# Kernel tuning notes

Measured on AMD Instinct MI355X. Metric: run time of the kernel, lower is better.

Reference implementation:

```python
import jax, jax.numpy as jnp
import numpy as np

B, C, H, W = 4, 1024, 14, 14
L = 80          # num labels / graph nodes
WD = 300        # word embedding dim
INTER = 1024    # semantic intermediary dim
OUT = 2048      # output_dim
TIME_STEP = 3


def setup_inputs() -> dict:
    key = jax.random.key(0)
    ks = jax.random.split(key, 24)
    s = 0.02  # weight scale to keep gates/tanh in sane range
    return {
        "img_feature_map": jax.random.normal(ks[0], (B, C, H, W), jnp.float32),
        "word_embedding": jax.random.normal(ks[1], (L, WD), jnp.float32),
        "adjacency": jax.random.uniform(ks[2], (L, L), jnp.float32) / L,
        "fc1_w": jax.random.normal(ks[3], (INTER, C), jnp.float32) * s,
        "fc2_w": jax.random.normal(ks[4], (INTER, WD), jnp.float32) * s,
        "fc3_w": jax.random.normal(ks[5], (INTER, INTER), jnp.float32) * s,
        "fc3_b": jnp.zeros((INTER,), jnp.float32),
        "fca_w": jax.random.normal(ks[6], (1, INTER), jnp.float32) * s,
        "fca_b": jnp.zeros((1,), jnp.float32),
        "w3": jax.random.normal(ks[7], (C, 2 * C), jnp.float32) * s,
        "b3": jnp.zeros((C,), jnp.float32),
        "u3": jax.random.normal(ks[8], (C, C), jnp.float32) * s,
        "u3b": jnp.zeros((C,), jnp.float32),
        "w4": jax.random.normal(ks[9], (C, 2 * C), jnp.float32) * s,
        "b4": jnp.zeros((C,), jnp.float32),
        "w5": jax.random.normal(ks[10], (C, 2 * C), jnp.float32) * s,
        "b5": jnp.zeros((C,), jnp.float32),
        "u5": jax.random.normal(ks[11], (C, C), jnp.float32) * s,
        "u5b": jnp.zeros((C,), jnp.float32),
        "fco_w": jax.random.normal(ks[12], (OUT, 2 * C), jnp.float32) * s,
        "fco_b": jnp.zeros((OUT,), jnp.float32),
    }


def _semantic(fmap, word_emb, fc1_w, fc2_w, fc3_w, fc3_b, fca_w, fca_b):
    # Faithful to torch: view(-1, C) on a contiguous (B,C,H,W) tensor is a raw
    # row-major reinterpret (NOT a BHWC transpose). jnp.reshape matches.
    b, c, h, w = fmap.shape
    x = fmap.reshape(-1, c)                                   # (B*H*W, C)
    f_wh = x @ fc1_w.T                                        # (N, INTER)
    f_wd = word_emb @ fc2_w.T                                 # (L, INTER)
    lb = jnp.tanh(f_wh[:, None, :] * f_wd[None, :, :])        # (N, L, INTER)
    lb = lb @ fc3_w.T + fc3_b                                 # (N, L, INTER)
    coeff = lb @ fca_w.T + fca_b                              # (N, L, 1)
    coeff = coeff.reshape(b, L, h * w)                        # torch .view semantics
    coeff = jax.nn.softmax(coeff, axis=2)
    coeff = coeff.reshape(b, h, w, L)
    fmap_bhwc = fmap.reshape(b, h, w, c)                      # raw reinterpret, as torch
    return jnp.einsum('bhwl,bhwc->blc', coeff, fmap_bhwc)     # (B, L, C)


def _ggnn(nodes, adj, w3, b3, u3, u3b, w4, b4, w5, b5, u5, u5b):
    for _ in range(TIME_STEP):
        a = jnp.einsum('nm,bmd->bnd', adj, nodes)             # in == out matrix
        av = jnp.concatenate([a, a], axis=-1)                 # (B, L, 2C)
        u3x = nodes @ u3.T + u3b
        z = jax.nn.sigmoid(av @ w3.T + b3 + u3x)
        r = jax.nn.sigmoid(av @ w4.T + b4 + u3x)              # torch bug: reuses fc_eq3_u
        hcand = jnp.tanh(av @ w5.T + b5 + (r * nodes) @ u5.T + u5b)
        nodes = (1.0 - z) * nodes + z * hcand
    return nodes


def reference(img_feature_map, word_embedding, adjacency,
              fc1_w, fc2_w, fc3_w, fc3_b, fca_w, fca_b,
              w3, b3, u3, u3b, w4, b4, w5, b5, u5, u5b,
              fco_w, fco_b):
    g = _semantic(img_feature_map, word_embedding,
                  fc1_w, fc2_w, fc3_w, fc3_b, fca_w, fca_b)   # (B, L, C)
    nodes = _ggnn(g, adjacency, w3, b3, u3, u3b, w4, b4, w5, b5, u5, u5b)
    feat = jnp.concatenate([nodes, g], axis=-1)               # (B, L, 2C)
    out = jnp.tanh(feat @ fco_w.T + fco_b)                    # (B, L, OUT)
    return out
```

## Files before the change

kernel.cpp:

```cpp
#include <hip/hip_runtime.h>
#include <hip/hip_bf16.h>

#define LL 80
#define NPIX 784
#define PBATCH 15680

#define DI __device__ __forceinline__

typedef short s8v __attribute__((ext_vector_type(8)));
typedef short short4v __attribute__((ext_vector_type(4)));
typedef float f32x4 __attribute__((ext_vector_type(4)));

DI float b2f(__hip_bfloat16 x) { return __bfloat162float(x); }
DI float s2f(short h) { return __uint_as_float(((unsigned int)(unsigned short)h) << 16); }

DI short f2b(float x) {
    unsigned int b = __float_as_uint(x);
    b += 0x7fffu + ((b >> 16) & 1u);
    return (short)(b >> 16);
}

template <int F> DI float LD(const void* p, int i) {
    if (F) return ((const float*)p)[i];
    return b2f(((const __hip_bfloat16*)p)[i]);
}

DI float fast_tanh(float x) {
    float e = __expf(2.0f * x);
    return 1.0f - 2.0f / (e + 1.0f);
}
DI float fast_sigmoid(float x) { return 1.0f / (1.0f + __expf(-x)); }

__global__ __launch_bounds__(256) void detect_dtype(const void* probe, int n, int* flag) {
    __shared__ int bad;
    if (threadIdx.x == 0) bad = 0;
    __syncthreads();
    int c = 0;
    for (int i = threadIdx.x; i < n; i += 256) {
        float v = b2f(((const __hip_bfloat16*)probe)[i]);
        if (!(fabsf(v) < 1000.0f)) c++;
    }
    if (c) atomicAdd(&bad, c);
    __syncthreads();
    if (threadIdx.x == 0) *flag = (bad > 8) ? 1 : 0;
}

DI void cvt_part(int f, const void* src, short* __restrict__ dst, int blk, int n) {
    int i0 = (blk * 256 + threadIdx.x) * 4;
    if (i0 >= n) return;
    if (f) {
        float4 v = *(const float4*)((const float*)src + i0);
        short4v o = { f2b(v.x), f2b(v.y), f2b(v.z), f2b(v.w) };
        *(short4v*)(dst + i0) = o;
    } else {
        *(short4v*)(dst + i0) = *(const short4v*)((const short*)src + i0);
    }
}

DI void wcat_part(int f, const void* w3, const void* w4, const void* w5, const void* u3,
                  short* __restrict__ wcat, int blk) {
    int i0 = (blk * 256 + threadIdx.x) * 4;
    int nr = i0 >> 10, k = i0 & 1023;
    int j = nr >> 10, r = nr & 1023;
    const void* W = (j == 0) ? w3 : (j == 1) ? w4 : (j == 2) ? w5 : u3;
    float4 v;
    if (j < 3) {
        if (f) {
            float4 x = *(const float4*)((const float*)W + r * 2048 + k);
            float4 y = *(const float4*)((const float*)W + r * 2048 + 1024 + k);
            v.x = x.x + y.x; v.y = x.y + y.y; v.z = x.z + y.z; v.w = x.w + y.w;
        } else {
            const short* Ws = (const short*)W;
            short4v x = *(const short4v*)(Ws + r * 2048 + k);
            short4v y = *(const short4v*)(Ws + r * 2048 + 1024 + k);
            v.x = s2f(x.x) + s2f(y.x); v.y = s2f(x.y) + s2f(y.y);
            v.z = s2f(x.z) + s2f(y.z); v.w = s2f(x.w) + s2f(y.w);
        }
    } else {
        if (f) v = *(const float4*)((const float*)W + r * 1024 + k);
        else {
            short4v x = *(const short4v*)((const short*)W + r * 1024 + k);
            v.x = s2f(x.x); v.y = s2f(x.y); v.z = s2f(x.z); v.w = s2f(x.w);
        }
    }
    short4v o = { f2b(v.x), f2b(v.y), f2b(v.z), f2b(v.w) };
    *(short4v*)(wcat + i0) = o;
}

template <int F>
DI void prep_u_part(const void* fc3_w, const void* fc3_b,
                    const void* fca_w, const void* fca_b,
                    float* u, float* c0, float* red, int blk) {
    if (blk < 4) {
        int k = blk * 256 + threadIdx.x;
        float acc = 0.f;
        for (int j = 0; j < 1024; j++)
            acc += LD<F>(fca_w, j) * LD<F>(fc3_w, j * 1024 + k);
        u[k] = acc;
    } else {
        float acc = 0.f;
        for (int j = threadIdx.x; j < 1024; j += 256)
            acc += LD<F>(fc3_b, j) * LD<F>(fca_w, j);
        red[threadIdx.x] = acc;
        __syncthreads();
        for (int s = 128; s > 0; s >>= 1) {
            if (threadIdx.x < s) red[threadIdx.x] += red[threadIdx.x + s];
            __syncthreads();
        }
        if (threadIdx.x == 0) *c0 = red[0] + LD<F>(fca_b, 0);
    }
}

template <int F>
DI void fc2_part(float* lds, const void* word, const void* fc2_w, float* C, int bx, int by) {
    float* As = lds;
    float* Ws2 = lds + 1088;
    const int tid = threadIdx.x;
    const int tx = tid & 15, ty = tid >> 4;
    const int m0 = by * 64, n0 = bx * 64;
    const int M = 80, K = 300;
    float acc[4][4] = {};

    for (int k0 = 0; k0 < K; k0 += 16) {
#pragma unroll
        for (int i = 0; i < 4; i++) {
            int idx = tid + i * 256;
            int kk = idx & 15, mm = idx >> 4;
            int m = m0 + mm, k = k0 + kk;
            As[kk * 68 + mm] = (m < M && k < K) ? LD<F>(word, m * 300 + k) : 0.f;
        }
#pragma unroll
        for (int i = 0; i < 4; i++) {
            int idx = tid + i * 256;
            int kk = idx & 15, nn = idx >> 4;
            int n = n0 + nn, k = k0 + kk;
            Ws2[kk * 68 + nn] = (k < K) ? LD<F>(fc2_w, n * 300 + k) : 0.f;
        }
        __syncthreads();
#pragma unroll
        for (int kk = 0; kk < 16; kk++) {
            float4 av = *(const float4*)(&As[kk * 68 + ty * 4]);
            float4 wv = *(const float4*)(&Ws2[kk * 68 + tx * 4]);
            float a4[4] = {av.x, av.y, av.z, av.w};
            float w4[4] = {wv.x, wv.y, wv.z, wv.w};
#pragma unroll
            for (int i = 0; i < 4; i++)
#pragma unroll
                for (int j = 0; j < 4; j++)
                    acc[i][j] += a4[i] * w4[j];
        }
        __syncthreads();
    }

    for (int i = 0; i < 4; i++) {
        int m = m0 + ty * 4 + i;
        if (m >= M) continue;
        for (int j = 0; j < 4; j++)
            C[m * 1024 + n0 + tx * 4 + j] = acc[i][j];
    }
}

__global__ __launch_bounds__(256) void mega_prep(
    const int* flag,
    const void* fmap, const void* fc1_w, const void* u5w,
    const void* w3, const void* w4, const void* w5, const void* u3,
    const void* fc3_w, const void* fc3_b, const void* fca_w, const void* fca_b,
    const void* word, const void* fc2_w,
    short* fmap_b, short* fc1w_b, short* u5w_b, short* wcat_b,
    float* u, float* c0, float* f_wd) {
    __shared__ float lds[2176];
    int f = *flag;
    int bid = blockIdx.x;
    if      (bid < 784)  cvt_part(f, fmap,  fmap_b, bid,        802816);
    else if (bid < 1808) cvt_part(f, fc1_w, fc1w_b, bid - 784,  1048576);
    else if (bid < 2832) cvt_part(f, u5w,   u5w_b,  bid - 1808, 1048576);
    else if (bid < 6928) wcat_part(f, w3, w4, w5, u3, wcat_b, bid - 2832);
    else if (bid < 6933) {
        if (f) prep_u_part<1>(fc3_w, fc3_b, fca_w, fca_b, u, c0, lds, bid - 6928);
        else   prep_u_part<0>(fc3_w, fc3_b, fca_w, fca_b, u, c0, lds, bid - 6928);
    } else {
        int r = bid - 6933;
        if (f) fc2_part<1>(lds, word, fc2_w, f_wd, r & 15, r >> 4);
        else   fc2_part<0>(lds, word, fc2_w, f_wd, r & 15, r >> 4);
    }
}

__global__ __launch_bounds__(256) void cvt_k(const int* flag, const void* src,
                                             short* __restrict__ dst, int n) {
    cvt_part(*flag, src, dst, blockIdx.x, n);
}

DI void mcore_b(const short* __restrict__ A, int lda,
                const short* __restrict__ B, int ldb,
                float* __restrict__ C, int ldc,
                int M, int kb, int ke, int m0, int n0) {
    __shared__ short As[4][64][8];
    __shared__ short Ws[4][64][8];
    const int tid = threadIdx.x;
    const int wv = tid >> 6, lane = tid & 63;
    const int mA = tid & 63, qA = tid >> 6;
    f32x4 acc[4] = {};

    for (int k0 = kb; k0 < ke; k0 += 32) {
        s8v va = {0,0,0,0,0,0,0,0};
        int gm = m0 + mA;
        if (gm < M) va = *(const s8v*)(A + gm * lda + k0 + 8 * qA);
        *(s8v*)&As[mA >> 4][(mA & 15) | (qA << 4)][0] = va;
        s8v vb = *(const s8v*)(B + (n0 + mA) * ldb + k0 + 8 * qA);
        *(s8v*)&Ws[mA >> 4][(mA & 15) | (qA << 4)][0] = vb;
        __syncthreads();
        s8v af = *(const s8v*)&As[wv][lane][0];
#pragma unroll
        for (int nf = 0; nf < 4; nf++) {
            s8v bf = *(const s8v*)&Ws[nf][lane][0];
            acc[nf] = __builtin_amdgcn_mfma_f32_16x16x32_bf16(af, bf, acc[nf], 0, 0, 0);
        }
        __syncthreads();
    }

    const int q = lane >> 4, cc = lane & 15;
#pragma unroll
    for (int nf = 0; nf < 4; nf++) {
        int n = n0 + 16 * nf + cc;
#pragma unroll
        for (int r = 0; r < 4; r++) {
            int m = m0 + 16 * wv + q * 4 + r;
            if (m < M) C[m * ldc + n] = acc[nf][r];
        }
    }
}

__global__ __launch_bounds__(256) void mfma_fc1(
    const short* __restrict__ fmap_b, const short* __restrict__ fc1w_b,
    float* __restrict__ fhP) {
    int z = blockIdx.z;
    mcore_b(fmap_b, 1024, fc1w_b, 1024, fhP + z * 802816, 1024,
            NPIX, z * 512, z * 512 + 512, blockIdx.y * 64, blockIdx.x * 64);
}

__global__ __launch_bounds__(256) void mfma_gate(
    const short* __restrict__ a_b, const short* __restrict__ nodes_b,
    const short* __restrict__ wcat_b, float* __restrict__ gP) {
    int z = blockIdx.z;
    const short* A = (blockIdx.x >= 48) ? nodes_b : a_b;
    mcore_b(A, 1024, wcat_b, 1024, gP + z * 1310720, 4096,
            320, z * 512, z * 512 + 512, blockIdx.y * 64, blockIdx.x * 64);
}

__global__ __launch_bounds__(256) void mfma_u5(
    const short* __restrict__ rn_b, const short* __restrict__ u5w_b,
    float* __restrict__ u5P) {
    int z = blockIdx.z;
    mcore_b(rn_b, 1024, u5w_b, 1024, u5P + z * 327680, 1024,
            320, z * 256, z * 256 + 256, blockIdx.y * 64, blockIdx.x * 64);
}

__global__ __launch_bounds__(256) void mfma_fin(
    const short* __restrict__ nodes_b, const short* __restrict__ g_b,
    const short* __restrict__ fcow_b, float* __restrict__ finP) {
    int z = blockIdx.z;
    const short* A = z ? (g_b - 1024) : nodes_b;
    mcore_b(A, 1024, fcow_b, 2048, finP + z * 655360, 2048,
            320, z * 1024, z * 1024 + 1024, blockIdx.y * 64, blockIdx.x * 64);
}

__global__ void fin_combine(const int* flag, const float* __restrict__ finP,
                            const void* fco_b, void* out, int n) {
    int i4 = (blockIdx.x * 256 + threadIdx.x) * 4;
    if (i4 >= n) return;
    int c = i4 & 2047;
    float4 p0 = *(const float4*)(finP + i4);
    float4 p1 = *(const float4*)(finP + 655360 + i4);
    int f = *flag;
    float v0 = fast_tanh(p0.x + p1.x + (f ? LD<1>(fco_b, c)   : LD<0>(fco_b, c)));
    float v1 = fast_tanh(p0.y + p1.y + (f ? LD<1>(fco_b, c+1) : LD<0>(fco_b, c+1)));
    float v2 = fast_tanh(p0.z + p1.z + (f ? LD<1>(fco_b, c+2) : LD<0>(fco_b, c+2)));
    float v3 = fast_tanh(p0.w + p1.w + (f ? LD<1>(fco_b, c+3) : LD<0>(fco_b, c+3)));
    if (f) {
        float4 o = {v0, v1, v2, v3};
        *(float4*)((float*)out + i4) = o;
    } else {
        short4v o = { f2b(v0), f2b(v1), f2b(v2), f2b(v3) };
        *(short4v*)((short*)out + i4) = o;
    }
}

__global__ __launch_bounds__(256) void coeff_kernel(
    const float* __restrict__ fhP, const float* __restrict__ f_wd,
    const float* __restrict__ u, const float* __restrict__ c0p,
    float* __restrict__ s) {
    int n = blockIdx.x;
    __shared__ float4 fh4[256];
    __shared__ float4 uu4[256];
    int t = threadIdx.x;
    {
        float4 a0 = *(const float4*)(fhP + n * 1024 + t * 4);
        float4 a1 = *(const float4*)(fhP + 802816 + n * 1024 + t * 4);
        float4 fv = {a0.x + a1.x, a0.y + a1.y, a0.z + a1.z, a0.w + a1.w};
        fh4[t] = fv;
        uu4[t] = *(const float4*)(u + t * 4);
    }
    __syncthreads();
    float c0 = *c0p;
    int wave = t >> 6, lane = t & 63;
    int b = n / 196, hw = n % 196;
    int l0 = blockIdx.y * 40;
    for (int l = l0 + wave; l < l0 + 40; l += 4) {
        const float4* fd4 = (const float4*)(f_wd + l * 1024);
        float p = 0.f;
#pragma unroll
        for (int k = 0; k < 4; k++) {
            int idx = lane + k * 64;
            float4 h = fh4[idx];
            float4 d = fd4[idx];
            float4 uu = uu4[idx];
            p += fast_tanh(h.x * d.x) * uu.x;
            p += fast_tanh(h.y * d.y) * uu.y;
            p += fast_tanh(h.z * d.z) * uu.z;
            p += fast_tanh(h.w * d.w) * uu.w;
        }
        for (int off = 32; off > 0; off >>= 1) p += __shfl_down(p, off);
        if (lane == 0) s[b * PBATCH + hw * LL + l] = p + c0;
    }
}

__global__ __launch_bounds__(64) void softmax196(float* __restrict__ s) {
    float* p = s + blockIdx.x * 196;
    int lane = threadIdx.x;
    float v[4];
    float mx = -1e30f;
#pragma unroll
    for (int i = 0; i < 4; i++) {
        int idx = lane + i * 64;
        v[i] = (idx < 196) ? p[idx] : -1e30f;
        mx = fmaxf(mx, v[i]);
    }
    for (int off = 32; off > 0; off >>= 1) mx = fmaxf(mx, __shfl_down(mx, off));
    mx = __shfl(mx, 0);
    float sum = 0.f;
#pragma unroll
    for (int i = 0; i < 4; i++) {
        int idx = lane + i * 64;
        if (idx < 196) { v[i] = __expf(v[i] - mx); sum += v[i]; }
    }
    for (int off = 32; off > 0; off >>= 1) sum += __shfl_down(sum, off);
    sum = __shfl(sum, 0);
    float inv = 1.f / sum;
#pragma unroll
    for (int i = 0; i < 4; i++) {
        int idx = lane + i * 64;
        if (idx < 196) p[idx] = v[i] * inv;
    }
}

__global__ __launch_bounds__(256) void g_kernel(
    const float* __restrict__ s, const short* __restrict__ fmap_b,
    float* __restrict__ nodes, short* __restrict__ nodes_b, short* __restrict__ g_b) {
    int bl = blockIdx.x;
    int b = bl / LL, l = bl % LL;
    __shared__ float co[196];
    for (int i = threadIdx.x; i < 196; i += 256)
        co[i] = s[b * PBATCH + i * LL + l];
    __syncthreads();
    int c4 = threadIdx.x * 4;
    const short* base = fmap_b + b * 196 * 1024 + c4;
    float a0 = 0.f, a1 = 0.f, a2 = 0.f, a3 = 0.f;
    for (int hw = 0; hw < 196; hw++) {
        short4v v = *(const short4v*)(base + hw * 1024);
        float w = co[hw];
        a0 += w * s2f(v.x); a1 += w * s2f(v.y);
        a2 += w * s2f(v.z); a3 += w * s2f(v.w);
    }
    int o = bl * 1024 + c4;
    float4 fa = {a0, a1, a2, a3};
    *(float4*)(nodes + o) = fa;
    short4v bb = { f2b(a0), f2b(a1), f2b(a2), f2b(a3) };
    *(short4v*)(nodes_b + o) = bb;
    *(short4v*)(g_b + o) = bb;
}

template <int F>
DI void adj_core(float* arw, const void* adj, const float* nodes, short* a_b) {
    int bl = blockIdx.x;
    int b = bl / LL, l = bl % LL;
    if (threadIdx.x < LL) arw[threadIdx.x] = LD<F>(adj, l * LL + threadIdx.x);
    __syncthreads();
    int c4 = threadIdx.x * 4;
    const float* nb = nodes + b * LL * 1024 + c4;
    float a0 = 0.f, a1 = 0.f, a2 = 0.f, a3 = 0.f;
    for (int m = 0; m < LL; m++) {
        float am = arw[m];
        float4 nd = *(const float4*)(nb + m * 1024);
        a0 += am * nd.x; a1 += am * nd.y; a2 += am * nd.z; a3 += am * nd.w;
    }
    short4v bb = { f2b(a0), f2b(a1), f2b(a2), f2b(a3) };
    *(short4v*)(a_b + bl * 1024 + c4) = bb;
}

__global__ __launch_bounds__(256) void adj_kernel(
    const int* flag, const void* adj, const float* nodes, short* a_b) {
    __shared__ float arw[LL];
    if (*flag) adj_core<1>(arw, adj, nodes, a_b);
    else       adj_core<0>(arw, adj, nodes, a_b);
}

template <int F>
DI void ew_r_core(const float* gP, const float* nodes,
                  const void* b4, const void* u3b, short* rn_b, int i4) {
    int m = i4 >> 10, c = i4 & 1023;
    int base = m * 4096;
    float4 r0 = *(const float4*)(gP + base + 1024 + c);
    float4 r1 = *(const float4*)(gP + 1310720 + base + 1024 + c);
    float4 x0 = *(const float4*)(gP + base + 3072 + c);
    float4 x1 = *(const float4*)(gP + 1310720 + base + 3072 + c);
    float4 nd = *(const float4*)(nodes + i4);
    short4v o;
    o.x = f2b(fast_sigmoid(r0.x + r1.x + x0.x + x1.x + LD<F>(b4, c)   + LD<F>(u3b, c))   * nd.x);
    o.y = f2b(fast_sigmoid(r0.y + r1.y + x0.y + x1.y + LD<F>(b4, c+1) + LD<F>(u3b, c+1)) * nd.y);
    o.z = f2b(fast_sigmoid(r0.z + r1.z + x0.z + x1.z + LD<F>(b4, c+2) + LD<F>(u3b, c+2)) * nd.z);
    o.w = f2b(fast_sigmoid(r0.w + r1.w + x0.w + x1.w + LD<F>(b4, c+3) + LD<F>(u3b, c+3)) * nd.w);
    *(short4v*)(rn_b + i4) = o;
}

__global__ void ew_r(const int* flag, const float* gP, const float* nodes,
                     const void* b4, const void* u3b, short* rn_b, int n) {
    int i4 = (blockIdx.x * 256 + threadIdx.x) * 4;
    if (i4 >= n) return;
    if (*flag) ew_r_core<1>(gP, nodes, b4, u3b, rn_b, i4);
    else       ew_r_core<0>(gP, nodes, b4, u3b, rn_b, i4);
}

template <int F>
DI void ewu(const float* gP, const float* u5P,
            const void* b3, const void* u3b, const void* b5, const void* u5b,
            float* nodes, short* nodes_b, int i4) {
    int m = i4 >> 10, c = i4 & 1023;
    int base = m * 4096;
    float4 z0 = *(const float4*)(gP + base + c);
    float4 z1 = *(const float4*)(gP + 1310720 + base + c);
    float4 h0 = *(const float4*)(gP + base + 2048 + c);
    float4 h1 = *(const float4*)(gP + 1310720 + base + 2048 + c);
    float4 x0 = *(const float4*)(gP + base + 3072 + c);
    float4 x1 = *(const float4*)(gP + 1310720 + base + 3072 + c);
    float4 u0 = *(const float4*)(u5P + i4);
    float4 u1 = *(const float4*)(u5P + 327680 + i4);
    float4 u2 = *(const float4*)(u5P + 655360 + i4);
    float4 u3v = *(const float4*)(u5P + 983040 + i4);
    float4 nd = *(const float4*)(nodes + i4);
    float4 out;
#define EWU1(CH, CO) { \
    float z = fast_sigmoid(z0.CH + z1.CH + x0.CH + x1.CH + LD<F>(b3, c+CO) + LD<F>(u3b, c+CO)); \
    float h = fast_tanh(h0.CH + h1.CH + u0.CH + u1.CH + u2.CH + u3v.CH + LD<F>(b5, c+CO) + LD<F>(u5b, c+CO)); \
    out.CH = (1.f - z) * nd.CH + z * h; }
    EWU1(x, 0) EWU1(y, 1) EWU1(z, 2) EWU1(w, 3)
#undef EWU1
    *(float4*)(nodes + i4) = out;
    short4v bb = { f2b(out.x), f2b(out.y), f2b(out.z), f2b(out.w) };
    *(short4v*)(nodes_b + i4) = bb;
}

__global__ void ew_upd(const int* flag, const float* gP, const float* u5P,
                       const void* b3, const void* u3b, const void* b5, const void* u5b,
                       float* nodes, short* nodes_b, int n) {
    int i4 = (blockIdx.x * 256 + threadIdx.x) * 4;
    if (i4 >= n) return;
    if (*flag) ewu<1>(gP, u5P, b3, u3b, b5, u5b, nodes, nodes_b, i4);
    else       ewu<0>(gP, u5P, b3, u3b, b5, u5b, nodes, nodes_b, i4);
}

extern "C" void kernel_launch(void* const* d_in, const int* in_sizes, int n_in,
                              void* d_out, int out_size, void* d_ws, size_t ws_size,
                              hipStream_t stream) {
    const void* fmap  = d_in[0];
    const void* word  = d_in[1];
    const void* adjm  = d_in[2];
    const void* fc1_w = d_in[3];
    const void* fc2_w = d_in[4];
    const void* fc3_w = d_in[5];
    const void* fc3_b = d_in[6];
    const void* fca_w = d_in[7];
    const void* fca_b = d_in[8];
    const void* w3    = d_in[9];
    const void* b3    = d_in[10];
    const void* u3    = d_in[11];
    const void* u3b   = d_in[12];
    const void* w4    = d_in[13];
    const void* b4    = d_in[14];
    const void* w5    = d_in[15];
    const void* b5    = d_in[16];
    const void* u5    = d_in[17];
    const void* u5b   = d_in[18];
    const void* fco_w = d_in[19];
    const void* fco_b = d_in[20];

    int*   flag    = (int*)d_ws;
    float* P       = (float*)d_ws + 16;
    float* nodes   = P;                       P += 327680;
    short* nodes_b = (short*)P;               P += 163840;
    short* g_b     = (short*)P;               P += 163840;
    short* a_b     = (short*)P;               P += 163840;
    short* rn_b    = (short*)P;               P += 163840;
    short* u5w_b   = (short*)P;               P += 524288;
    short* wcat_b  = (short*)P;               P += 2097152;
    float* R       = P;
    float* fhP    = R;
    float* f_wd   = R + 1605632;
    float* u      = f_wd + 81920;
    float* c0     = u + 1024;
    float* s      = c0 + 16;
    short* fmap_b = (short*)(s + 62720);
    short* fc1w_b = (short*)(s + 62720 + 401408);
    float* gP     = R;
    float* u5P    = R + 2621440;
    float* finP   = R;
    short* fcow_b = (short*)(R + 1310720);

    detect_dtype<<<1, 256, 0, stream>>>(fc1_w, 4096, flag);

    mega_prep<<<6965, 256, 0, stream>>>(flag, fmap, fc1_w, u5,
                                        w3, w4, w5, u3,
                                        fc3_w, fc3_b, fca_w, fca_b,
                                        word, fc2_w,
                                        fmap_b, fc1w_b, u5w_b, wcat_b,
                                        u, c0, f_wd);

    mfma_fc1<<<dim3(16, 13, 2), 256, 0, stream>>>(fmap_b, fc1w_b, fhP);
    coeff_kernel<<<dim3(NPIX, 2), 256, 0, stream>>>(fhP, f_wd, u, c0, s);
    softmax196<<<320, 64, 0, stream>>>(s);
    g_kernel<<<320, 256, 0, stream>>>(s, fmap_b, nodes, nodes_b, g_b);

    for (int t = 0; t < 3; t++) {
        adj_kernel<<<320, 256, 0, stream>>>(flag, adjm, nodes, a_b);
        mfma_gate<<<dim3(64, 5, 2), 256, 0, stream>>>(a_b, nodes_b, wcat_b, gP);
        ew_r<<<320, 256, 0, stream>>>(flag, gP, nodes, b4, u3b, rn_b, 327680);
        mfma_u5<<<dim3(16, 5, 4), 256, 0, stream>>>(rn_b, u5w_b, u5P);
        ew_upd<<<320, 256, 0, stream>>>(flag, gP, u5P, b3, u3b, b5, u5b,
                                        nodes, nodes_b, 327680);
    }

    cvt_k<<<4096, 256, 0, stream>>>(flag, fco_w, fcow_b, 4194304);
    mfma_fin<<<dim3(32, 5, 2), 256, 0, stream>>>(nodes_b, g_b, fcow_b, finP);
    fin_combine<<<640, 256, 0, stream>>>(flag, finP, fco_b, d_out, 655360);
}
```

Before: 393.2 us.

## Fuse GRU update and final tanh into MFMA epilogues; parallelize u prep

The u5 GEMM now applies the GRU update (sigmoid, tanh, blend, bf16 write) in its epilogue, and the final fco GEMM applies bias and tanh directly to the output. Both GEMMs drop their split-K partial buffers and the separate elementwise kernels. The fco_w conversion moves into the mega_prep launch, and the u-vector prep is split into 16 row-chunk blocks with vectorized loads that coeff_kernel sums. Without split-K the fused GEMMs launch far fewer blocks (80 and 160), so they may run with lower parallelism and longer per-block K loops.

Result: slower. 439.0 us (+11.7%).

```diff
diff --git a/kernel.cpp b/kernel.cpp
--- a/kernel.cpp
+++ b/kernel.cpp
@@ -24,6 +24,7 @@
     if (F) return ((const float*)p)[i];
     return b2f(((const __hip_bfloat16*)p)[i]);
 }
+DI float LDf(int f, const void* p, int i) { return f ? ((const float*)p)[i] : b2f(((const __hip_bfloat16*)p)[i]); }
 
 DI float fast_tanh(float x) {
     float e = __expf(2.0f * x);
@@ -88,27 +89,36 @@
 }
 
 template <int F>
-DI void prep_u_part(const void* fc3_w, const void* fc3_b,
-                    const void* fca_w, const void* fca_b,
-                    float* u, float* c0, float* red, int blk) {
-    if (blk < 4) {
-        int k = blk * 256 + threadIdx.x;
-        float acc = 0.f;
-        for (int j = 0; j < 1024; j++)
-            acc += LD<F>(fca_w, j) * LD<F>(fc3_w, j * 1024 + k);
-        u[k] = acc;
-    } else {
-        float acc = 0.f;
-        for (int j = threadIdx.x; j < 1024; j += 256)
-            acc += LD<F>(fc3_b, j) * LD<F>(fca_w, j);
-        red[threadIdx.x] = acc;
-        __syncthreads();
-        for (int s = 128; s > 0; s >>= 1) {
-            if (threadIdx.x < s) red[threadIdx.x] += red[threadIdx.x + s];
-            __syncthreads();
-        }
-        if (threadIdx.x == 0) *c0 = red[0] + LD<F>(fca_b, 0);
-    }
+DI void u_part(const void* fc3_w, const void* fca_w, float* __restrict__ uP, int jsplit) {
+    int k4 = threadIdx.x * 4;
+    float4 acc = {0.f, 0.f, 0.f, 0.f};
+    for (int j = jsplit * 64; j < jsplit * 64 + 64; j++) {
+        float fa = LD<F>(fca_w, j);
+        float4 row;
+        if (F) row = *(const float4*)((const float*)fc3_w + j * 1024 + k4);
+        else {
+            short4v x = *(const short4v*)((const short*)fc3_w + j * 1024 + k4);
+            row.x = s2f(x.x); row.y = s2f(x.y); row.z = s2f(x.z); row.w = s2f(x.w);
+        }
+        acc.x += fa * row.x; acc.y += fa * row.y;
+        acc.z += fa * row.z; acc.w += fa * row.w;
+    }
+    *(float4*)(uP + jsplit * 1024 + k4) = acc;
+}
+
+template <int F>
+DI void c0_part(const void* fc3_b, const void* fca_w, const void* fca_b,
+                float* c0, float* red) {
+    float acc = 0.f;
+    for (int j = threadIdx.x; j < 1024; j += 256)
+        acc += LD<F>(fc3_b, j) * LD<F>(fca_w, j);
+    red[threadIdx.x] = acc;
+    __syncthreads();
+    for (int s = 128; s > 0; s >>= 1) {
+        if (threadIdx.x < s) red[threadIdx.x] += red[threadIdx.x + s];
+        __syncthreads();
+    }
+    if (threadIdx.x == 0) *c0 = red[0] + LD<F>(fca_b, 0);
 }
 
 template <int F>
@@ -162,32 +172,31 @@
 
 __global__ __launch_bounds__(256) void mega_prep(
     const int* flag,
-    const void* fmap, const void* fc1_w, const void* u5w,
+    const void* fmap, const void* fc1_w, const void* u5w, const void* fco_w,
     const void* w3, const void* w4, const void* w5, const void* u3,
     const void* fc3_w, const void* fc3_b, const void* fca_w, const void* fca_b,
     const void* word, const void* fc2_w,
-    short* fmap_b, short* fc1w_b, short* u5w_b, short* wcat_b,
-    float* u, float* c0, float* f_wd) {
+    short* fmap_b, short* fc1w_b, short* u5w_b, short* wcat_b, short* fcow_b,
+    float* uP, float* c0, float* f_wd) {
     __shared__ float lds[2176];
     int f = *flag;
     int bid = blockIdx.x;
-    if      (bid < 784)  cvt_part(f, fmap,  fmap_b, bid,        802816);
-    else if (bid < 1808) cvt_part(f, fc1_w, fc1w_b, bid - 784,  1048576);
-    else if (bid < 2832) cvt_part(f, u5w,   u5w_b,  bid - 1808, 1048576);
-    else if (bid < 6928) wcat_part(f, w3, w4, w5, u3, wcat_b, bid - 2832);
-    else if (bid < 6933) {
-        if (f) prep_u_part<1>(fc3_w, fc3_b, fca_w, fca_b, u, c0, lds, bid - 6928);
-        else   prep_u_part<0>(fc3_w, fc3_b, fca_w, fca_b, u, c0, lds, bid - 6928);
-    } else {
-        int r = bid - 6933;
+    if (bid < 16) {
+        if (f) u_part<1>(fc3_w, fca_w, uP, bid);
+        else   u_part<0>(fc3_w, fca_w, uP, bid);
+    } else if (bid == 16) {
+        if (f) c0_part<1>(fc3_b, fca_w, fca_b, c0, lds);
+        else   c0_part<0>(fc3_b, fca_w, fca_b, c0, lds);
+    } else if (bid < 49) {
+        int r = bid - 17;
         if (f) fc2_part<1>(lds, word, fc2_w, f_wd, r & 15, r >> 4);
         else   fc2_part<0>(lds, word, fc2_w, f_wd, r & 15, r >> 4);
     }
-}
-
-__global__ __launch_bounds__(256) void cvt_k(const int* flag, const void* src,
-                                             short* __restrict__ dst, int n) {
-    cvt_part(*flag, src, dst, blockIdx.x, n);
+    else if (bid < 833)  cvt_part(f, fmap,  fmap_b, bid - 49,   802816);
+    else if (bid < 1857) cvt_part(f, fc1_w, fc1w_b, bid - 833,  1048576);
+    else if (bid < 2881) cvt_part(f, u5w,   u5w_b,  bid - 1857, 1048576);
+    else if (bid < 6977) wcat_part(f, w3, w4, w5, u3, wcat_b, bid - 2881);
+    else                 cvt_part(f, fco_w, fcow_b, bid - 6977, 4194304);
 }
 
 DI void mcore_b(const short* __restrict__ A, int lda,
@@ -247,47 +256,103 @@
             320, z * 512, z * 512 + 512, blockIdx.y * 64, blockIdx.x * 64);
 }
 
-__global__ __launch_bounds__(256) void mfma_u5(
-    const short* __restrict__ rn_b, const short* __restrict__ u5w_b,
-    float* __restrict__ u5P) {
-    int z = blockIdx.z;
-    mcore_b(rn_b, 1024, u5w_b, 1024, u5P + z * 327680, 1024,
-            320, z * 256, z * 256 + 256, blockIdx.y * 64, blockIdx.x * 64);
-}
-
-__global__ __launch_bounds__(256) void mfma_fin(
-    const short* __restrict__ nodes_b, const short* __restrict__ g_b,
-    const short* __restrict__ fcow_b, float* __restrict__ finP) {
-    int z = blockIdx.z;
-    const short* A = z ? (g_b - 1024) : nodes_b;
-    mcore_b(A, 1024, fcow_b, 2048, finP + z * 655360, 2048,
-            320, z * 1024, z * 1024 + 1024, blockIdx.y * 64, blockIdx.x * 64);
-}
-
-__global__ void fin_combine(const int* flag, const float* __restrict__ finP,
-                            const void* fco_b, void* out, int n) {
-    int i4 = (blockIdx.x * 256 + threadIdx.x) * 4;
-    if (i4 >= n) return;
-    int c = i4 & 2047;
-    float4 p0 = *(const float4*)(finP + i4);
-    float4 p1 = *(const float4*)(finP + 655360 + i4);
-    int f = *flag;
-    float v0 = fast_tanh(p0.x + p1.x + (f ? LD<1>(fco_b, c)   : LD<0>(fco_b, c)));
-    float v1 = fast_tanh(p0.y + p1.y + (f ? LD<1>(fco_b, c+1) : LD<0>(fco_b, c+1)));
-    float v2 = fast_tanh(p0.z + p1.z + (f ? LD<1>(fco_b, c+2) : LD<0>(fco_b, c+2)));
-    float v3 = fast_tanh(p0.w + p1.w + (f ? LD<1>(fco_b, c+3) : LD<0>(fco_b, c+3)));
-    if (f) {
-        float4 o = {v0, v1, v2, v3};
-        *(float4*)((float*)out + i4) = o;
-    } else {
-        short4v o = { f2b(v0), f2b(v1), f2b(v2), f2b(v3) };
-        *(short4v*)((short*)out + i4) = o;
+__global__ __launch_bounds__(256) void mfma_u5f(
+    const int* flag, const short* __restrict__ rn_b, const short* __restrict__ u5w_b,
+    const float* __restrict__ gP,
+    const void* b3, const void* u3b, const void* b5, const void* u5b,
+    float* __restrict__ nodes, short* __restrict__ nodes_b) {
+    __shared__ short As[4][64][8];
+    __shared__ short Ws[4][64][8];
+    const int tid = threadIdx.x;
+    const int wv = tid >> 6, lane = tid & 63;
+    const int mA = tid & 63, qA = tid >> 6;
+    const int m0 = blockIdx.y * 64, n0 = blockIdx.x * 64;
+    f32x4 acc[4] = {};
+
+    for (int k0 = 0; k0 < 1024; k0 += 32) {
+        s8v va = *(const s8v*)(rn_b + (m0 + mA) * 1024 + k0 + 8 * qA);
+        *(s8v*)&As[mA >> 4][(mA & 15) | (qA << 4)][0] = va;
+        s8v vb = *(const s8v*)(u5w_b + (n0 + mA) * 1024 + k0 + 8 * qA);
+        *(s8v*)&Ws[mA >> 4][(mA & 15) | (qA << 4)][0] = vb;
+        __syncthreads();
+        s8v af = *(const s8v*)&As[wv][lane][0];
+#pragma unroll
+        for (int nf = 0; nf < 4; nf++) {
+            s8v bf = *(const s8v*)&Ws[nf][lane][0];
+            acc[nf] = __builtin_amdgcn_mfma_f32_16x16x32_bf16(af, bf, acc[nf], 0, 0, 0);
+        }
+        __syncthreads();
+    }
+
+    const int f = *flag;
+    const int q = lane >> 4, cc = lane & 15;
+#pragma unroll
+    for (int nf = 0; nf < 4; nf++) {
+        int n = n0 + 16 * nf + cc;
+        float bb3 = LDf(f, b3, n), bu3 = LDf(f, u3b, n);
+        float bb5 = LDf(f, b5, n), bu5 = LDf(f, u5b, n);
+#pragma unroll
+        for (int r = 0; r < 4; r++) {
+            int m = m0 + 16 * wv + q * 4 + r;
+            int i = m * 1024 + n, base = m * 4096;
+            float az = gP[base + n]        + gP[1310720 + base + n];
+            float ah = gP[base + 2048 + n] + gP[1310720 + base + 2048 + n];
+            float ux = gP[base + 3072 + n] + gP[1310720 + base + 3072 + n];
+            float z = fast_sigmoid(az + ux + bb3 + bu3);
+            float h = fast_tanh(ah + acc[nf][r] + bb5 + bu5);
+            float nd = (1.f - z) * nodes[i] + z * h;
+            nodes[i] = nd;
+            nodes_b[i] = f2b(nd);
+        }
+    }
+}
+
+__global__ __launch_bounds__(256) void mfma_finf(
+    const int* flag, const short* __restrict__ nodes_b, const short* __restrict__ g_b,
+    const short* __restrict__ fcow_b, const void* fco_b, void* out) {
+    __shared__ short As[4][64][8];
+    __shared__ short Ws[4][64][8];
+    const int tid = threadIdx.x;
+    const int wv = tid >> 6, lane = tid & 63;
+    const int mA = tid & 63, qA = tid >> 6;
+    const int m0 = blockIdx.y * 64, n0 = blockIdx.x * 64;
+    f32x4 acc[4] = {};
+
+    for (int k0 = 0; k0 < 2048; k0 += 32) {
+        const short* Ap = (k0 < 1024) ? nodes_b : (g_b - 1024);
+        s8v va = *(const s8v*)(Ap + (m0 + mA) * 1024 + k0 + 8 * qA);
+        *(s8v*)&As[mA >> 4][(mA & 15) | (qA << 4)][0] = va;
+        s8v vb = *(const s8v*)(fcow_b + (n0 + mA) * 2048 + k0 + 8 * qA);
+        *(s8v*)&Ws[mA >> 4][(mA & 15) | (qA << 4)][0] = vb;
+        __syncthreads();
+        s8v af = *(const s8v*)&As[wv][lane][0];
+#pragma unroll
+        for (int nf = 0; nf < 4; nf++) {
+            s8v bf = *(const s8v*)&Ws[nf][lane][0];
+            acc[nf] = __builtin_amdgcn_mfma_f32_16x16x32_bf16(af, bf, acc[nf], 0, 0, 0);
+        }
+        __syncthreads();
+    }
+
+    const int f = *flag;
+    const int q = lane >> 4, cc = lane & 15;
+#pragma unroll
+    for (int nf = 0; nf < 4; nf++) {
+        int n = n0 + 16 * nf + cc;
+        float bias = LDf(f, fco_b, n);
+#pragma unroll
+        for (int r = 0; r < 4; r++) {
+            int m = m0 + 16 * wv + q * 4 + r;
+            float v = fast_tanh(acc[nf][r] + bias);
+            if (f) ((float*)out)[m * 2048 + n] = v;
+            else   ((__hip_bfloat16*)out)[m * 2048 + n] = __float2bfloat16(v);
+        }
     }
 }
 
 __global__ __launch_bounds__(256) void coeff_kernel(
     const float* __restrict__ fhP, const float* __restrict__ f_wd,
-    const float* __restrict__ u, const float* __restrict__ c0p,
+    const float* __restrict__ uP, const float* __restrict__ c0p,
     float* __restrict__ s) {
     int n = blockIdx.x;
     __shared__ float4 fh4[256];
@@ -298,7 +363,12 @@
         float4 a1 = *(const float4*)(fhP + 802816 + n * 1024 + t * 4);
         float4 fv = {a0.x + a1.x, a0.y + a1.y, a0.z + a1.z, a0.w + a1.w};
         fh4[t] = fv;
-        uu4[t] = *(const float4*)(u + t * 4);
+        float4 uv = {0.f, 0.f, 0.f, 0.f};
+        for (int p = 0; p < 16; p++) {
+            float4 q4 = *(const float4*)(uP + p * 1024 + t * 4);
+            uv.x += q4.x; uv.y += q4.y; uv.z += q4.z; uv.w += q4.w;
+        }
+        uu4[t] = uv;
     }
     __syncthreads();
     float c0 = *c0p;
@@ -428,44 +498,6 @@
     if (i4 >= n) return;
     if (*flag) ew_r_core<1>(gP, nodes, b4, u3b, rn_b, i4);
     else       ew_r_core<0>(gP, nodes, b4, u3b, rn_b, i4);
-}
-
-template <int F>
-DI void ewu(const float* gP, const float* u5P,
-            const void* b3, const void* u3b, const void* b5, const void* u5b,
-            float* nodes, short* nodes_b, int i4) {
-    int m = i4 >> 10, c = i4 & 1023;
-    int base = m * 4096;
-    float4 z0 = *(const float4*)(gP + base + c);
-    float4 z1 = *(const float4*)(gP + 1310720 + base + c);
-    float4 h0 = *(const float4*)(gP + base + 2048 + c);
-    float4 h1 = *(const float4*)(gP + 1310720 + base + 2048 + c);
-    float4 x0 = *(const float4*)(gP + base + 3072 + c);
-    float4 x1 = *(const float4*)(gP + 1310720 + base + 3072 + c);
-    float4 u0 = *(const float4*)(u5P + i4);
-    float4 u1 = *(const float4*)(u5P + 327680 + i4);
-    float4 u2 = *(const float4*)(u5P + 655360 + i4);
-    float4 u3v = *(const float4*)(u5P + 983040 + i4);
-    float4 nd = *(const float4*)(nodes + i4);
-    float4 out;
-#define EWU1(CH, CO) { \
-    float z = fast_sigmoid(z0.CH + z1.CH + x0.CH + x1.CH + LD<F>(b3, c+CO) + LD<F>(u3b, c+CO)); \
-    float h = fast_tanh(h0.CH + h1.CH + u0.CH + u1.CH + u2.CH + u3v.CH + LD<F>(b5, c+CO) + LD<F>(u5b, c+CO)); \
-    out.CH = (1.f - z) * nd.CH + z * h; }
-    EWU1(x, 0) EWU1(y, 1) EWU1(z, 2) EWU1(w, 3)
-#undef EWU1
-    *(float4*)(nodes + i4) = out;
-    short4v bb = { f2b(out.x), f2b(out.y), f2b(out.z), f2b(out.w) };
-    *(short4v*)(nodes_b + i4) = bb;
-}
-
-__global__ void ew_upd(const int* flag, const float* gP, const float* u5P,
-                       const void* b3, const void* u3b, const void* b5, const void* u5b,
-                       float* nodes, short* nodes_b, int n) {
-    int i4 = (blockIdx.x * 256 + threadIdx.x) * 4;
-    if (i4 >= n) return;
-    if (*flag) ewu<1>(gP, u5P, b3, u3b, b5, u5b, nodes, nodes_b, i4);
-    else       ewu<0>(gP, u5P, b3, u3b, b5, u5b, nodes, nodes_b, i4);
 }
 
 extern "C" void kernel_launch(void* const* d_in, const int* in_sizes, int n_in,
@@ -505,27 +537,25 @@
     float* R       = P;
     float* fhP    = R;
     float* f_wd   = R + 1605632;
-    float* u      = f_wd + 81920;
-    float* c0     = u + 1024;
+    float* uP     = f_wd + 81920;
+    float* c0     = uP + 16384;
     float* s      = c0 + 16;
     short* fmap_b = (short*)(s + 62720);
     short* fc1w_b = (short*)(s + 62720 + 401408);
+    short* fcow_b = (short*)(R + 2692368);
     float* gP     = R;
-    float* u5P    = R + 2621440;
-    float* finP   = R;
-    short* fcow_b = (short*)(R + 1310720);
 
     detect_dtype<<<1, 256, 0, stream>>>(fc1_w, 4096, flag);
 
-    mega_prep<<<6965, 256, 0, stream>>>(flag, fmap, fc1_w, u5,
-                                        w3, w4, w5, u3,
-                                        fc3_w, fc3_b, fca_w, fca_b,
-                                        word, fc2_w,
-                                        fmap_b, fc1w_b, u5w_b, wcat_b,
-                                        u, c0, f_wd);
+    mega_prep<<<11073, 256, 0, stream>>>(flag, fmap, fc1_w, u5, fco_w,
+                                         w3, w4, w5, u3,
+                                         fc3_w, fc3_b, fca_w, fca_b,
+                                         word, fc2_w,
+                                         fmap_b, fc1w_b, u5w_b, wcat_b, fcow_b,
+                                         uP, c0, f_wd);
 
     mfma_fc1<<<dim3(16, 13, 2), 256, 0, stream>>>(fmap_b, fc1w_b, fhP);
-    coeff_kernel<<<dim3(NPIX, 2), 256, 0, stream>>>(fhP, f_wd, u, c0, s);
+    coeff_kernel<<<dim3(NPIX, 2), 256, 0, stream>>>(fhP, f_wd, uP, c0, s);
     softmax196<<<320, 64, 0, stream>>>(s);
     g_kernel<<<320, 256, 0, stream>>>(s, fmap_b, nodes, nodes_b, g_b);
 
@@ -533,12 +563,9 @@
         adj_kernel<<<320, 256, 0, stream>>>(flag, adjm, nodes, a_b);
         mfma_gate<<<dim3(64, 5, 2), 256, 0, stream>>>(a_b, nodes_b, wcat_b, gP);
         ew_r<<<320, 256, 0, stream>>>(flag, gP, nodes, b4, u3b, rn_b, 327680);
-        mfma_u5<<<dim3(16, 5, 4), 256, 0, stream>>>(rn_b, u5w_b, u5P);
-        ew_upd<<<320, 256, 0, stream>>>(flag, gP, u5P, b3, u3b, b5, u5b,
-                                        nodes, nodes_b, 327680);
-    }
-
-    cvt_k<<<4096, 256, 0, stream>>>(flag, fco_w, fcow_b, 4194304);
-    mfma_fin<<<dim3(32, 5, 2), 256, 0, stream>>>(nodes_b, g_b, fcow_b, finP);
-    fin_combine<<<640, 256, 0, stream>>>(flag, finP, fco_b, d_out, 655360);
-}
+        mfma_u5f<<<dim3(16, 5), 256, 0, stream>>>(flag, rn_b, u5w_b, gP,
+                                                  b3, u3b, b5, u5b, nodes, nodes_b);
+    }
+
+    mfma_finf<<<dim3(32, 5), 256, 0, stream>>>(flag, nodes_b, g_b, fcow_b, fco_b, d_out);
+}
```
